# Performance work log

Measured on AMD Instinct MI355X. Metric: run time of the kernel, lower is better.

The kernel has to match this reference:

```python
import jax, jax.numpy as jnp
import numpy as np
from jax import lax

# --- block geometry (matches init_kwargs) ---
B = 8
DIM = 192
HEADS = 6
KEY_DIM = DIM // HEADS  # 32, attn_ratio=1 so d == key_dim and dh == DIM
HX, WX = 32, 32         # search region
HZ, WZ = 16, 16         # template region
T = 1                   # template_number
L = HX * WX + T * HZ * WZ  # 1280 tokens
MLP_HIDDEN = int(DIM * 4.0)
BN_EPS = 1e-5


def _build_bias_idx():
    """Replicates Attention.__init__ global_att=True bias-index construction.
    Unique-offset ids may be permuted vs torch dict-insertion order, which is an
    equivalent reparameterization of the (randomly initialized) bias table."""
    g = np.stack(np.meshgrid(np.arange(HX), np.arange(WX), indexing='ij'), -1).reshape(-1, 2)
    pts = [g]
    for i in range(T):
        r = np.arange(HX + HZ * i, WX + WZ * (i + 1))
        g2 = np.stack(np.meshgrid(r, r, indexing='ij'), -1).reshape(-1, 2)
        pts.append(g2)
    p = np.concatenate(pts, 0)                      # (L, 2)
    off = np.abs(p[:, None, :] - p[None, :, :])     # (L, L, 2)
    key = off[:, :, 0].astype(np.int64) * 4096 + off[:, :, 1]
    uniq, inv = np.unique(key, return_inverse=True)
    return inv.reshape(L, L).astype(np.int32), int(len(uniq))


def setup_inputs() -> dict:
    key = jax.random.key(0)
    ks = jax.random.split(key, 16)
    idx_np, n_off = _build_bias_idx()
    s = 0.02
    return {
        'xz': jax.random.normal(ks[0], (B, L, DIM), jnp.float32),
        'bias_idx': jnp.asarray(idx_np),
        'ln1_g': jnp.ones((DIM,), jnp.float32),
        'ln1_b': jnp.zeros((DIM,), jnp.float32),
        'wqkv': jax.random.normal(ks[1], (DIM, 3 * DIM), jnp.float32) * s,
        'bqkv': jnp.zeros((3 * DIM,), jnp.float32),
        'wproj': jax.random.normal(ks[2], (DIM, DIM), jnp.float32) * s,
        'bproj': jnp.zeros((DIM,), jnp.float32),
        'bias_table': jax.random.normal(ks[3], (HEADS, n_off), jnp.float32) * 0.1,
        'conv_w': jax.random.normal(ks[4], (3, 3, 1, DIM), jnp.float32) * 0.1,  # depthwise HWIO
        'bn_scale': jnp.ones((DIM,), jnp.float32) + jax.random.normal(ks[5], (DIM,), jnp.float32) * 0.01,
        'bn_bias': jax.random.normal(ks[6], (DIM,), jnp.float32) * 0.01,
        'ln2_g': jnp.ones((DIM,), jnp.float32),
        'ln2_b': jnp.zeros((DIM,), jnp.float32),
        'w1': jax.random.normal(ks[7], (DIM, MLP_HIDDEN), jnp.float32) * s,
        'b1': jnp.zeros((MLP_HIDDEN,), jnp.float32),
        'w2': jax.random.normal(ks[8], (MLP_HIDDEN, DIM), jnp.float32) * s,
        'b2': jnp.zeros((DIM,), jnp.float32),
    }


def _layernorm(x, g, b, eps=1e-5):
    mu = jnp.mean(x, -1, keepdims=True)
    var = jnp.mean(jnp.square(x - mu), -1, keepdims=True)
    return (x - mu) * lax.rsqrt(var + eps) * g + b


def reference(xz, bias_idx, ln1_g, ln1_b, wqkv, bqkv, wproj, bproj, bias_table,
              conv_w, bn_scale, bn_bias, ln2_g, ln2_b, w1, b1, w2, b2):
    Bn, N, D = xz.shape
    scale = KEY_DIM ** -0.5
    # --- Attention (LeViT-style with gathered relative-position bias) ---
    h = _layernorm(xz, ln1_g, ln1_b)
    qkv = (h @ wqkv + bqkv).reshape(Bn, N, HEADS, 3 * KEY_DIM)
    q, k, v = jnp.split(qkv, 3, axis=3)            # each (B, N, H, key_dim)
    bias = bias_table[:, bias_idx]                  # (H, N, N) gather
    attn = jnp.einsum('bnhd,bmhd->bhnm', q, k) * scale + bias
    attn = jax.nn.softmax(attn, axis=-1)
    o = jnp.einsum('bhnm,bmhd->bnhd', attn, v).reshape(Bn, N, D)
    xm = xz + o @ wproj + bproj
    # --- depthwise local conv (Conv2d_BN, BN folded to scale/bias) per segment ---
    segs = []
    start = 0
    for (Hh, Ww) in [(HX, WX)] + [(HZ, WZ)] * T:
        xc = xm[:, start:start + Hh * Ww, :].reshape(Bn, Hh, Ww, D)
        xc = lax.conv_general_dilated(
            xc, conv_w, window_strides=(1, 1), padding='SAME',
            dimension_numbers=('NHWC', 'HWIO', 'NHWC'), feature_group_count=D)
        xc = xc * bn_scale + bn_bias
        segs.append(xc.reshape(Bn, Hh * Ww, D))
        start += Hh * Ww
    xm = jnp.concatenate(segs, axis=1)
    # --- MLP with pre-LN (exact GELU, matching nn.GELU default) ---
    m = _layernorm(xm, ln2_g, ln2_b)
    m = jax.nn.gelu(m @ w1 + b1, approximate=False) @ w2 + b2
    return xm + m
```

## Files before the change

kernel.cpp:

```cpp
#include <hip/hip_runtime.h>
#include <hip/hip_bf16.h>

#define BATCH 8
#define LTOK 1280
#define DIMC 192
#define HEADS 6
#define KD 32
#define HID 768
#define NROWS (BATCH*LTOK)

typedef short s16x8 __attribute__((ext_vector_type(8)));
typedef float f32x4 __attribute__((ext_vector_type(4)));
typedef unsigned short u16;

#define QS (0.17677669529663687f * 1.4426950408889634f)
#define L2E 1.4426950408889634f

__device__ __forceinline__ u16 f2bf(float x) {
    unsigned u = __float_as_uint(x);
    u = (u + 0x7FFFu + ((u >> 16) & 1u)) >> 16;
    return (u16)u;
}
__device__ __forceinline__ float bflo(unsigned u) { return __uint_as_float(u << 16); }
__device__ __forceinline__ float bfhi(unsigned u) { return __uint_as_float(u & 0xffff0000u); }
__device__ __forceinline__ float fexp2(float x) { float r; asm("v_exp_f32 %0, %1" : "=v"(r) : "v"(x)); return r; }
__device__ __forceinline__ float frcp(float x)  { float r; asm("v_rcp_f32 %0, %1" : "=v"(r) : "v"(x)); return r; }

__global__ __launch_bounds__(256) void ln_kernel(const float* __restrict__ x,
                                                 const float* __restrict__ g,
                                                 const float* __restrict__ b,
                                                 u16* __restrict__ y) {
    int row = blockIdx.x * 4 + (threadIdx.x >> 6);
    int lane = threadIdx.x & 63;
    const float* xr = x + (size_t)row * DIMC;
    float v0 = xr[lane], v1 = xr[lane + 64], v2 = xr[lane + 128];
    float s = v0 + v1 + v2;
    float ss = v0 * v0 + v1 * v1 + v2 * v2;
    #pragma unroll
    for (int off = 32; off; off >>= 1) {
        s  += __shfl_xor(s, off);
        ss += __shfl_xor(ss, off);
    }
    float mu  = s * (1.0f / DIMC);
    float var = ss * (1.0f / DIMC) - mu * mu;
    float inv = rsqrtf(var + 1e-5f);
    u16* yr = y + (size_t)row * DIMC;
    yr[lane]       = f2bf((v0 - mu) * inv * g[lane]       + b[lane]);
    yr[lane + 64]  = f2bf((v1 - mu) * inv * g[lane + 64]  + b[lane + 64]);
    yr[lane + 128] = f2bf((v2 - mu) * inv * g[lane + 128] + b[lane + 128]);
}

__global__ __launch_bounds__(256) void pre_kernel(const float* w0, const float* w1,
                                                  const float* w2, const float* w3,
                                                  u16* o0, u16* o1, u16* o2, u16* o3,
                                                  const int* __restrict__ bidx,
                                                  const float* __restrict__ btab,
                                                  int n_off, u16* __restrict__ bm) {
    __shared__ float s[16][17];
    int f = blockIdx.x;
    if (f >= 1728) {
        size_t flat = (size_t)(f - 1728) * 1024 + (size_t)threadIdx.x * 4;
        int4 iv = *(const int4*)(bidx + flat);
        #pragma unroll
        for (int h = 0; h < HEADS; ++h) {
            const float* tab = btab + (size_t)h * n_off;
            ushort4 o;
            o.x = f2bf(tab[iv.x] * L2E);
            o.y = f2bf(tab[iv.y] * L2E);
            o.z = f2bf(tab[iv.z] * L2E);
            o.w = f2bf(tab[iv.w] * L2E);
            *(ushort4*)(bm + (size_t)h * (LTOK * LTOK) + flat) = o;
        }
        return;
    }
    const float* in; u16* out; int K, N, tn, tk;
    if (f < 432)       { in = w0; out = o0; K = 192; N = 576; int r = f;        tn = r % 36; tk = r / 36; }
    else if (f < 576)  { in = w1; out = o1; K = 192; N = 192; int r = f - 432;  tn = r % 12; tk = r / 12; }
    else if (f < 1152) { in = w2; out = o2; K = 192; N = 768; int r = f - 576;  tn = r % 48; tk = r / 48; }
    else               { in = w3; out = o3; K = 768; N = 192; int r = f - 1152; tn = r % 12; tk = r / 12; }
    int tx = threadIdx.x & 15, ty = threadIdx.x >> 4;
    s[ty][tx] = in[(size_t)(tk * 16 + ty) * N + tn * 16 + tx];
    __syncthreads();
    out[(size_t)(tn * 16 + ty) * K + tk * 16 + tx] = f2bf(s[tx][ty]);
}

template<int ACT, int RES, int OBF, int QKV, int K, int MTILE>
__global__ __launch_bounds__(256) void gemm_mfma(const u16* __restrict__ A,
                                                 const u16* __restrict__ Wt,
                                                 const float* __restrict__ bias,
                                                 const float* __restrict__ R,
                                                 void* __restrict__ Cp,
                                                 u16* __restrict__ qb,
                                                 u16* __restrict__ kp,
                                                 u16* __restrict__ vp,
                                                 int N) {
    constexpr int SUB = MTILE / 64;
    int tid = threadIdx.x;
    int L = tid & 63, w = tid >> 6;
    int r = L & 15, g = L >> 4;
    int m0 = blockIdx.y * MTILE + w * (16 * SUB);
    int n0 = blockIdx.x * 64;

    f32x4 acc[SUB][4] = {};
    const u16* Ab = A + (size_t)(m0 + r) * K + g * 8;
    const u16* Wb = Wt + (size_t)(n0 + r) * K + g * 8;
    #pragma unroll 6
    for (int k0 = 0; k0 < K; k0 += 32) {
        s16x8 af[SUB];
        #pragma unroll
        for (int mi = 0; mi < SUB; ++mi)
            af[mi] = *(const s16x8*)(Ab + (size_t)mi * 16 * K + k0);
        #pragma unroll
        for (int nn = 0; nn < 4; ++nn) {
            s16x8 bf = *(const s16x8*)(Wb + (size_t)nn * 16 * K + k0);
            #pragma unroll
            for (int mi = 0; mi < SUB; ++mi)
                acc[mi][nn] = __builtin_amdgcn_mfma_f32_16x16x32_bf16(af[mi], bf, acc[mi][nn], 0, 0, 0);
        }
    }

    #pragma unroll
    for (int mi = 0; mi < SUB; ++mi)
    #pragma unroll
    for (int nn = 0; nn < 4; ++nn) {
        int cb = n0 + nn * 16;
        #pragma unroll
        for (int i = 0; i < 4; ++i) {
            int row = m0 + mi * 16 + g * 4 + i;
            float v = acc[mi][nn][i] + bias[cb + r];
            if (QKV) {
                int h  = cb / 96, c0 = cb % 96;
                int reg = c0 >> 5;
                if (reg == 0) {
                    v *= QS;
                    qb[(size_t)row * DIMC + h * 32 + (c0 & 31) + r] = f2bf(v);
                } else {
                    int b_ = row / LTOK, t = row - b_ * LTOK;
                    int T = t >> 5, it = t & 31;
                    int d = (c0 & 31) + r;
                    if (reg == 1) {
                        int which = (it >> 2) & 1;
                        int ik = ((it >> 3) << 2) | (it & 3);
                        int Lk = ((d >> 3) << 4) + ik;
                        kp[((size_t)(b_ * HEADS + h) * 40 + T) * 1024 + which * 512 + Lk * 8 + (d & 7)] = f2bf(v);
                    } else {
                        int Lv = ((it >> 3) << 4) + (d & 15);
                        vp[((size_t)(b_ * HEADS + h) * 40 + T) * 1024 + (d >> 4) * 512 + Lv * 8 + (it & 7)] = f2bf(v);
                    }
                }
            } else {
                if (ACT == 1) {
                    float u = v;
                    float y = 0.7978845608028654f * (u + 0.044715f * u * u * u);
                    float e2 = fexp2(y * 2.885390081777927f);
                    v = u - u * frcp(e2 + 1.0f);
                }
                if (RES) v += R[(size_t)row * N + cb + r];
                if (OBF) ((u16*)Cp)[(size_t)row * N + cb + r] = f2bf(v);
                else     ((float*)Cp)[(size_t)row * N + cb + r] = v;
            }
        }
    }
}

__global__ __launch_bounds__(256) void attn_mfma(const u16* __restrict__ qb,
                                                 const u16* __restrict__ kp,
                                                 const u16* __restrict__ vp,
                                                 const u16* __restrict__ bm,
                                                 u16* __restrict__ ob) {
    __shared__ __align__(16) u16 kvs[3][2][1024];
    int tid = threadIdx.x;
    int L = tid & 63, w = tid >> 6;
    int r = L & 15, g = L >> 4;
    int L8 = L * 8;

    int bid = blockIdx.x;
    int work = (bid & 7) * 120 + (bid >> 3);
    int b  = work & 7;
    int hq = work >> 3;
    int qt = (hq % 20) * 4 + w;
    int h  = hq / 20;

    s16x8 qf = *(const s16x8*)(qb + (size_t)(b * LTOK + qt * 16 + r) * DIMC + h * 32 + g * 8);

    int skv = w >> 1, half = w & 1;
    const u16* gsrc = (skv ? vp : kp) + (size_t)(b * HEADS + h) * 40 * 1024 + half * 512 + L8;
    u16* kvsb = &kvs[0][0][0];
    int dofs = skv * 1024 + half * 512 + L8;

    const u16* bmr = bm + ((size_t)h * LTOK + qt * 16 + r) * LTOK + g * 8;

    f32x4 acc0 = {0.f, 0.f, 0.f, 0.f}, acc1 = {0.f, 0.f, 0.f, 0.f};
    float lsum = 0.f;

    int4 st0 = *(const int4*)(gsrc);
    *(int4*)(kvsb + dofs) = st0;
    int4 sCur = *(const int4*)(gsrc + 1024);
    int4 bv  = *(const int4*)(bmr);
    int4 bvn = *(const int4*)(bmr + 32);
    __syncthreads();

    int rd = 0, wr = 1;
    #pragma unroll 1
    for (int T = 0; T < 40; ++T) {
        int4 sNext, bb;
        if (T < 38) {
            sNext = *(const int4*)(gsrc + (size_t)(T + 2) * 1024);
            bb    = *(const int4*)(bmr + (size_t)(T + 2) * 32);
        }
        u16* bufr = kvsb + rd * 2048;
        f32x4 z0, z1;
        z0[0] = bflo(bv.x); z0[1] = bfhi(bv.x); z0[2] = bflo(bv.y); z0[3] = bfhi(bv.y);
        z1[0] = bflo(bv.z); z1[1] = bfhi(bv.z); z1[2] = bflo(bv.w); z1[3] = bfhi(bv.w);

        s16x8 kf0 = *(const s16x8*)(bufr + L8);
        s16x8 kf1 = *(const s16x8*)(bufr + 512 + L8);
        __builtin_amdgcn_s_setprio(1);
        f32x4 s0 = __builtin_amdgcn_mfma_f32_16x16x32_bf16(kf0, qf, z0, 0, 0, 0);
        f32x4 s1 = __builtin_amdgcn_mfma_f32_16x16x32_bf16(kf1, qf, z1, 0, 0, 0);
        float p[8];
        #pragma unroll
        for (int j = 0; j < 4; ++j) p[j] = fexp2(s0[j]);
        #pragma unroll
        for (int j = 0; j < 4; ++j) p[4 + j] = fexp2(s1[j]);
        lsum += ((p[0] + p[1]) + (p[2] + p[3])) + ((p[4] + p[5]) + (p[6] + p[7]));
        union { unsigned u[4]; s16x8 v; } pbu;
        #pragma unroll
        for (int j = 0; j < 4; ++j)
            asm("v_cvt_pk_bf16_f32 %0, %1, %2" : "=v"(pbu.u[j]) : "v"(p[2 * j]), "v"(p[2 * j + 1]));
        s16x8 v0 = *(const s16x8*)(bufr + 1024 + L8);
        s16x8 v1 = *(const s16x8*)(bufr + 1536 + L8);
        acc0 = __builtin_amdgcn_mfma_f32_16x16x32_bf16(pbu.v, v0, acc0, 0, 0, 0);
        acc1 = __builtin_amdgcn_mfma_f32_16x16x32_bf16(pbu.v, v1, acc1, 0, 0, 0);
        __builtin_amdgcn_s_setprio(0);

        if (T < 39) *(int4*)(kvsb + wr * 2048 + dofs) = sCur;
        __syncthreads();
        sCur = sNext; bv = bvn; bvn = bb;
        rd = wr; wr = (wr == 2) ? 0 : wr + 1;
    }

    float lr = lsum;
    lr += __shfl_xor(lr, 16);
    lr += __shfl_xor(lr, 32);
    #pragma unroll
    for (int i = 0; i < 4; ++i) {
        float linv = frcp(__shfl(lr, 4 * g + i));
        size_t orow = (size_t)(b * LTOK + qt * 16 + 4 * g + i) * DIMC + h * 32 + r;
        ob[orow]      = f2bf(acc0[i] * linv);
        ob[orow + 16] = f2bf(acc1[i] * linv);
    }
}

__global__ __launch_bounds__(256) void conv_ln_kernel(const float* __restrict__ xm,
                                                      const float* __restrict__ w,
                                                      const float* __restrict__ scale,
                                                      const float* __restrict__ bias,
                                                      const float* __restrict__ g2,
                                                      const float* __restrict__ b2,
                                                      float* __restrict__ xm2,
                                                      u16* __restrict__ y) {
    int row = blockIdx.x * 4 + (threadIdx.x >> 6);
    int lane = threadIdx.x & 63;
    int b = row / LTOK, t = row - b * LTOK;
    int H, W, base, y0, x0;
    if (t < 1024) { H = 32; W = 32; base = 0;    y0 = t >> 5;            x0 = t & 31; }
    else          { H = 16; W = 16; base = 1024; int tt = t - 1024; y0 = tt >> 4; x0 = tt & 15; }
    float a0 = 0.f, a1 = 0.f, a2 = 0.f;
    #pragma unroll
    for (int ky = 0; ky < 3; ++ky) {
        int yy = y0 + ky - 1;
        if (yy < 0 || yy >= H) continue;
        #pragma unroll
        for (int kx = 0; kx < 3; ++kx) {
            int xx = x0 + kx - 1;
            if (xx < 0 || xx >= W) continue;
            const float* xr = xm + (size_t)(b * LTOK + base + yy * W + xx) * DIMC;
            const float* wr = w + (ky * 3 + kx) * DIMC;
            a0 += wr[lane]       * xr[lane];
            a1 += wr[lane + 64]  * xr[lane + 64];
            a2 += wr[lane + 128] * xr[lane + 128];
        }
    }
    float v0 = a0 * scale[lane]       + bias[lane];
    float v1 = a1 * scale[lane + 64]  + bias[lane + 64];
    float v2 = a2 * scale[lane + 128] + bias[lane + 128];
    float* xr2 = xm2 + (size_t)row * DIMC;
    xr2[lane] = v0; xr2[lane + 64] = v1; xr2[lane + 128] = v2;
    float s = v0 + v1 + v2;
    float ss = v0 * v0 + v1 * v1 + v2 * v2;
    #pragma unroll
    for (int off = 32; off; off >>= 1) {
        s  += __shfl_xor(s, off);
        ss += __shfl_xor(ss, off);
    }
    float mu  = s * (1.0f / DIMC);
    float var = ss * (1.0f / DIMC) - mu * mu;
    float inv = rsqrtf(var + 1e-5f);
    u16* yr = y + (size_t)row * DIMC;
    yr[lane]       = f2bf((v0 - mu) * inv * g2[lane]       + b2[lane]);
    yr[lane + 64]  = f2bf((v1 - mu) * inv * g2[lane + 64]  + b2[lane + 64]);
    yr[lane + 128] = f2bf((v2 - mu) * inv * g2[lane + 128] + b2[lane + 128]);
}

extern "C" void kernel_launch(void* const* d_in, const int* in_sizes, int n_in,
                              void* d_out, int out_size, void* d_ws, size_t ws_size,
                              hipStream_t stream) {
    const float* xz       = (const float*)d_in[0];
    const int*   bidx     = (const int*)  d_in[1];
    const float* ln1_g    = (const float*)d_in[2];
    const float* ln1_b    = (const float*)d_in[3];
    const float* wqkv     = (const float*)d_in[4];
    const float* bqkv     = (const float*)d_in[5];
    const float* wproj    = (const float*)d_in[6];
    const float* bproj    = (const float*)d_in[7];
    const float* btab     = (const float*)d_in[8];
    const float* conv_w   = (const float*)d_in[9];
    const float* bn_scale = (const float*)d_in[10];
    const float* bn_bias  = (const float*)d_in[11];
    const float* ln2_g    = (const float*)d_in[12];
    const float* ln2_b    = (const float*)d_in[13];
    const float* w1       = (const float*)d_in[14];
    const float* b1       = (const float*)d_in[15];
    const float* w2       = (const float*)d_in[16];
    const float* b2       = (const float*)d_in[17];
    int n_off = in_sizes[8] / HEADS;
    float* out = (float*)d_out;

    char* wsb = (char*)d_ws;
    u16*  hbuf   = (u16*)(wsb + 0);
    u16*  ob     = (u16*)(wsb + 0);
    u16*  wqkvT  = (u16*)(wsb + 3932160);
    u16*  wprojT = (u16*)(wsb + 4153344);
    u16*  w1T    = (u16*)(wsb + 4227072);
    u16*  w2T    = (u16*)(wsb + 4521984);
    u16*  bm     = (u16*)(wsb + 4816896);
    u16*  hid    = (u16*)(wsb + 4816896);
    u16*  kp     = (u16*)(wsb + 24477696);
    u16*  vp     = (u16*)(wsb + 28409856);
    float* xm2   = (float*)(wsb + 24477696);
    u16*  qb     = (u16*)(wsb + 32342016);
    float* xm    = (float*)(wsb + 32342016);

    pre_kernel<<<1728 + LTOK * LTOK / 1024, 256, 0, stream>>>(
        wqkv, wproj, w1, w2, wqkvT, wprojT, w1T, w2T, bidx, btab, n_off, bm);
    ln_kernel<<<NROWS / 4, 256, 0, stream>>>(xz, ln1_g, ln1_b, hbuf);
    gemm_mfma<0,0,0,1,DIMC,128><<<dim3(576 / 64, NROWS / 128), 256, 0, stream>>>(
        hbuf, wqkvT, bqkv, nullptr, nullptr, qb, kp, vp, 3 * DIMC);
    attn_mfma<<<960, 256, 0, stream>>>(qb, kp, vp, bm, ob);
    gemm_mfma<0,1,0,0,DIMC,64><<<dim3(DIMC / 64, NROWS / 64), 256, 0, stream>>>(
        ob, wprojT, bproj, xz, xm, nullptr, nullptr, nullptr, DIMC);
    conv_ln_kernel<<<NROWS / 4, 256, 0, stream>>>(
        xm, conv_w, bn_scale, bn_bias, ln2_g, ln2_b, xm2, hbuf);
    gemm_mfma<1,0,1,0,DIMC,128><<<dim3(HID / 64, NROWS / 128), 256, 0, stream>>>(
        hbuf, w1T, b1, nullptr, hid, nullptr, nullptr, nullptr, HID);
    gemm_mfma<0,1,0,0,HID,128><<<dim3(DIMC / 64, NROWS / 128), 256, 0, stream>>>(
        hid, w2T, b2, xm2, out, nullptr, nullptr, nullptr, DIMC);
}
```

Measured before the change: 136.0 us.

## Fuse LN1 into pre kernel, double KV tile per attention step, retune GEMM tiles

```diff
diff --git a/kernel.cpp b/kernel.cpp
--- a/kernel.cpp
+++ b/kernel.cpp
@@ -26,38 +26,39 @@
 __device__ __forceinline__ float fexp2(float x) { float r; asm("v_exp_f32 %0, %1" : "=v"(r) : "v"(x)); return r; }
 __device__ __forceinline__ float frcp(float x)  { float r; asm("v_rcp_f32 %0, %1" : "=v"(r) : "v"(x)); return r; }
 
-__global__ __launch_bounds__(256) void ln_kernel(const float* __restrict__ x,
-                                                 const float* __restrict__ g,
-                                                 const float* __restrict__ b,
-                                                 u16* __restrict__ y) {
-    int row = blockIdx.x * 4 + (threadIdx.x >> 6);
-    int lane = threadIdx.x & 63;
-    const float* xr = x + (size_t)row * DIMC;
-    float v0 = xr[lane], v1 = xr[lane + 64], v2 = xr[lane + 128];
-    float s = v0 + v1 + v2;
-    float ss = v0 * v0 + v1 * v1 + v2 * v2;
-    #pragma unroll
-    for (int off = 32; off; off >>= 1) {
-        s  += __shfl_xor(s, off);
-        ss += __shfl_xor(ss, off);
-    }
-    float mu  = s * (1.0f / DIMC);
-    float var = ss * (1.0f / DIMC) - mu * mu;
-    float inv = rsqrtf(var + 1e-5f);
-    u16* yr = y + (size_t)row * DIMC;
-    yr[lane]       = f2bf((v0 - mu) * inv * g[lane]       + b[lane]);
-    yr[lane + 64]  = f2bf((v1 - mu) * inv * g[lane + 64]  + b[lane + 64]);
-    yr[lane + 128] = f2bf((v2 - mu) * inv * g[lane + 128] + b[lane + 128]);
-}
-
 __global__ __launch_bounds__(256) void pre_kernel(const float* w0, const float* w1,
                                                   const float* w2, const float* w3,
                                                   u16* o0, u16* o1, u16* o2, u16* o3,
                                                   const int* __restrict__ bidx,
                                                   const float* __restrict__ btab,
-                                                  int n_off, u16* __restrict__ bm) {
+                                                  int n_off, u16* __restrict__ bm,
+                                                  const float* __restrict__ xz,
+                                                  const float* __restrict__ ln1g,
+                                                  const float* __restrict__ ln1b,
+                                                  u16* __restrict__ hbuf) {
     __shared__ float s[16][17];
     int f = blockIdx.x;
+    if (f >= 3328) {
+        int row = (f - 3328) * 4 + (threadIdx.x >> 6);
+        int lane = threadIdx.x & 63;
+        const float* xr = xz + (size_t)row * DIMC;
+        float v0 = xr[lane], v1 = xr[lane + 64], v2 = xr[lane + 128];
+        float sm = v0 + v1 + v2;
+        float ss = v0 * v0 + v1 * v1 + v2 * v2;
+        #pragma unroll
+        for (int off = 32; off; off >>= 1) {
+            sm += __shfl_xor(sm, off);
+            ss += __shfl_xor(ss, off);
+        }
+        float mu  = sm * (1.0f / DIMC);
+        float var = ss * (1.0f / DIMC) - mu * mu;
+        float inv = rsqrtf(var + 1e-5f);
+        u16* yr = hbuf + (size_t)row * DIMC;
+        yr[lane]       = f2bf((v0 - mu) * inv * ln1g[lane]       + ln1b[lane]);
+        yr[lane + 64]  = f2bf((v1 - mu) * inv * ln1g[lane + 64]  + ln1b[lane + 64]);
+        yr[lane + 128] = f2bf((v2 - mu) * inv * ln1g[lane + 128] + ln1b[lane + 128]);
+        return;
+    }
     if (f >= 1728) {
         size_t flat = (size_t)(f - 1728) * 1024 + (size_t)threadIdx.x * 4;
         int4 iv = *(const int4*)(bidx + flat);
@@ -168,7 +169,7 @@
                                                  const u16* __restrict__ vp,
                                                  const u16* __restrict__ bm,
                                                  u16* __restrict__ ob) {
-    __shared__ __align__(16) u16 kvs[3][2][1024];
+    __shared__ __align__(16) u16 kvs[2][2][2048];
     int tid = threadIdx.x;
     int L = tid & 63, w = tid >> 6;
     int r = L & 15, g = L >> 4;
@@ -184,60 +185,85 @@
     s16x8 qf = *(const s16x8*)(qb + (size_t)(b * LTOK + qt * 16 + r) * DIMC + h * 32 + g * 8);
 
     int skv = w >> 1, half = w & 1;
-    const u16* gsrc = (skv ? vp : kp) + (size_t)(b * HEADS + h) * 40 * 1024 + half * 512 + L8;
-    u16* kvsb = &kvs[0][0][0];
-    int dofs = skv * 1024 + half * 512 + L8;
+    const u16* gs = (skv ? vp : kp) + (size_t)(b * HEADS + h) * 40 * 1024 + L8;
+    u16* dst0 = &kvs[0][skv][half * 1024 + L8];
+    u16* dst1 = &kvs[1][skv][half * 1024 + L8];
 
     const u16* bmr = bm + ((size_t)h * LTOK + qt * 16 + r) * LTOK + g * 8;
 
     f32x4 acc0 = {0.f, 0.f, 0.f, 0.f}, acc1 = {0.f, 0.f, 0.f, 0.f};
     float lsum = 0.f;
 
-    int4 st0 = *(const int4*)(gsrc);
-    *(int4*)(kvsb + dofs) = st0;
-    int4 sCur = *(const int4*)(gsrc + 1024);
-    int4 bv  = *(const int4*)(bmr);
-    int4 bvn = *(const int4*)(bmr + 32);
+    {
+        int4 pA = *(const int4*)(gs + half * 1024);
+        int4 pB = *(const int4*)(gs + half * 1024 + 512);
+        *(int4*)dst0 = pA;
+        *(int4*)(dst0 + 512) = pB;
+    }
+    int4 bv0 = *(const int4*)(bmr);
+    int4 bv1 = *(const int4*)(bmr + 32);
     __syncthreads();
 
-    int rd = 0, wr = 1;
     #pragma unroll 1
-    for (int T = 0; T < 40; ++T) {
-        int4 sNext, bb;
-        if (T < 38) {
-            sNext = *(const int4*)(gsrc + (size_t)(T + 2) * 1024);
-            bb    = *(const int4*)(bmr + (size_t)(T + 2) * 32);
-        }
-        u16* bufr = kvsb + rd * 2048;
-        f32x4 z0, z1;
-        z0[0] = bflo(bv.x); z0[1] = bfhi(bv.x); z0[2] = bflo(bv.y); z0[3] = bfhi(bv.y);
-        z1[0] = bflo(bv.z); z1[1] = bfhi(bv.z); z1[2] = bflo(bv.w); z1[3] = bfhi(bv.w);
-
-        s16x8 kf0 = *(const s16x8*)(bufr + L8);
-        s16x8 kf1 = *(const s16x8*)(bufr + 512 + L8);
+    for (int T = 0; T < 20; ++T) {
+        int4 nA, nB, nb0, nb1;
+        if (T < 19) {
+            nA  = *(const int4*)(gs + (size_t)(2 * T + 2 + half) * 1024);
+            nB  = *(const int4*)(gs + (size_t)(2 * T + 2 + half) * 1024 + 512);
+            nb0 = *(const int4*)(bmr + (size_t)(T + 1) * 64);
+            nb1 = *(const int4*)(bmr + (size_t)(T + 1) * 64 + 32);
+        }
+        const u16* kb = &kvs[T & 1][0][0];
+        const u16* vb = &kvs[T & 1][1][0];
+        f32x4 z0, z1, z2, z3;
+        z0[0] = bflo(bv0.x); z0[1] = bfhi(bv0.x); z0[2] = bflo(bv0.y); z0[3] = bfhi(bv0.y);
+        z1[0] = bflo(bv0.z); z1[1] = bfhi(bv0.z); z1[2] = bflo(bv0.w); z1[3] = bfhi(bv0.w);
+        z2[0] = bflo(bv1.x); z2[1] = bfhi(bv1.x); z2[2] = bflo(bv1.y); z2[3] = bfhi(bv1.y);
+        z3[0] = bflo(bv1.z); z3[1] = bfhi(bv1.z); z3[2] = bflo(bv1.w); z3[3] = bfhi(bv1.w);
+
+        s16x8 kf0 = *(const s16x8*)(kb + L8);
+        s16x8 kf1 = *(const s16x8*)(kb + 512 + L8);
+        s16x8 kf2 = *(const s16x8*)(kb + 1024 + L8);
+        s16x8 kf3 = *(const s16x8*)(kb + 1536 + L8);
         __builtin_amdgcn_s_setprio(1);
         f32x4 s0 = __builtin_amdgcn_mfma_f32_16x16x32_bf16(kf0, qf, z0, 0, 0, 0);
         f32x4 s1 = __builtin_amdgcn_mfma_f32_16x16x32_bf16(kf1, qf, z1, 0, 0, 0);
-        float p[8];
-        #pragma unroll
-        for (int j = 0; j < 4; ++j) p[j] = fexp2(s0[j]);
-        #pragma unroll
-        for (int j = 0; j < 4; ++j) p[4 + j] = fexp2(s1[j]);
-        lsum += ((p[0] + p[1]) + (p[2] + p[3])) + ((p[4] + p[5]) + (p[6] + p[7]));
-        union { unsigned u[4]; s16x8 v; } pbu;
-        #pragma unroll
-        for (int j = 0; j < 4; ++j)
-            asm("v_cvt_pk_bf16_f32 %0, %1, %2" : "=v"(pbu.u[j]) : "v"(p[2 * j]), "v"(p[2 * j + 1]));
-        s16x8 v0 = *(const s16x8*)(bufr + 1024 + L8);
-        s16x8 v1 = *(const s16x8*)(bufr + 1536 + L8);
-        acc0 = __builtin_amdgcn_mfma_f32_16x16x32_bf16(pbu.v, v0, acc0, 0, 0, 0);
-        acc1 = __builtin_amdgcn_mfma_f32_16x16x32_bf16(pbu.v, v1, acc1, 0, 0, 0);
+        f32x4 s2 = __builtin_amdgcn_mfma_f32_16x16x32_bf16(kf2, qf, z2, 0, 0, 0);
+        f32x4 s3 = __builtin_amdgcn_mfma_f32_16x16x32_bf16(kf3, qf, z3, 0, 0, 0);
+        float p[16];
+        #pragma unroll
+        for (int j = 0; j < 4; ++j) {
+            p[j]      = fexp2(s0[j]);
+            p[4 + j]  = fexp2(s1[j]);
+            p[8 + j]  = fexp2(s2[j]);
+            p[12 + j] = fexp2(s3[j]);
+        }
+        float t0 = ((p[0] + p[1]) + (p[2] + p[3])) + ((p[4] + p[5]) + (p[6] + p[7]));
+        float t1 = ((p[8] + p[9]) + (p[10] + p[11])) + ((p[12] + p[13]) + (p[14] + p[15]));
+        lsum += t0 + t1;
+        union { unsigned u[4]; s16x8 v; } pa, pb;
+        #pragma unroll
+        for (int j = 0; j < 4; ++j) {
+            asm("v_cvt_pk_bf16_f32 %0, %1, %2" : "=v"(pa.u[j]) : "v"(p[2 * j]), "v"(p[2 * j + 1]));
+            asm("v_cvt_pk_bf16_f32 %0, %1, %2" : "=v"(pb.u[j]) : "v"(p[8 + 2 * j]), "v"(p[9 + 2 * j]));
+        }
+        s16x8 v0 = *(const s16x8*)(vb + L8);
+        s16x8 v1 = *(const s16x8*)(vb + 512 + L8);
+        s16x8 v2 = *(const s16x8*)(vb + 1024 + L8);
+        s16x8 v3 = *(const s16x8*)(vb + 1536 + L8);
+        acc0 = __builtin_amdgcn_mfma_f32_16x16x32_bf16(pa.v, v0, acc0, 0, 0, 0);
+        acc1 = __builtin_amdgcn_mfma_f32_16x16x32_bf16(pa.v, v1, acc1, 0, 0, 0);
+        acc0 = __builtin_amdgcn_mfma_f32_16x16x32_bf16(pb.v, v2, acc0, 0, 0, 0);
+        acc1 = __builtin_amdgcn_mfma_f32_16x16x32_bf16(pb.v, v3, acc1, 0, 0, 0);
         __builtin_amdgcn_s_setprio(0);
 
-        if (T < 39) *(int4*)(kvsb + wr * 2048 + dofs) = sCur;
+        if (T < 19) {
+            u16* d = (T & 1) ? dst0 : dst1;
+            *(int4*)d = nA;
+            *(int4*)(d + 512) = nB;
+            bv0 = nb0; bv1 = nb1;
+        }
         __syncthreads();
-        sCur = sNext; bv = bvn; bvn = bb;
-        rd = wr; wr = (wr == 2) ? 0 : wr + 1;
     }
 
     float lr = lsum;
@@ -342,17 +368,17 @@
     u16*  qb     = (u16*)(wsb + 32342016);
     float* xm    = (float*)(wsb + 32342016);
 
-    pre_kernel<<<1728 + LTOK * LTOK / 1024, 256, 0, stream>>>(
-        wqkv, wproj, w1, w2, wqkvT, wprojT, w1T, w2T, bidx, btab, n_off, bm);
-    ln_kernel<<<NROWS / 4, 256, 0, stream>>>(xz, ln1_g, ln1_b, hbuf);
-    gemm_mfma<0,0,0,1,DIMC,128><<<dim3(576 / 64, NROWS / 128), 256, 0, stream>>>(
+    pre_kernel<<<1728 + LTOK * LTOK / 1024 + NROWS / 4, 256, 0, stream>>>(
+        wqkv, wproj, w1, w2, wqkvT, wprojT, w1T, w2T, bidx, btab, n_off, bm,
+        xz, ln1_g, ln1_b, hbuf);
+    gemm_mfma<0,0,0,1,DIMC,256><<<dim3(576 / 64, NROWS / 256), 256, 0, stream>>>(
         hbuf, wqkvT, bqkv, nullptr, nullptr, qb, kp, vp, 3 * DIMC);
     attn_mfma<<<960, 256, 0, stream>>>(qb, kp, vp, bm, ob);
-    gemm_mfma<0,1,0,0,DIMC,64><<<dim3(DIMC / 64, NROWS / 64), 256, 0, stream>>>(
+    gemm_mfma<0,1,0,0,DIMC,128><<<dim3(DIMC / 64, NROWS / 128), 256, 0, stream>>>(
         ob, wprojT, bproj, xz, xm, nullptr, nullptr, nullptr, DIMC);
     conv_ln_kernel<<<NROWS / 4, 256, 0, stream>>>(
         xm, conv_w, bn_scale, bn_bias, ln2_g, ln2_b, xm2, hbuf);
-    gemm_mfma<1,0,1,0,DIMC,128><<<dim3(HID / 64, NROWS / 128), 256, 0, stream>>>(
+    gemm_mfma<1,0,1,0,DIMC,256><<<dim3(HID / 64, NROWS / 256), 256, 0, stream>>>(
         hbuf, w1T, b1, nullptr, hid, nullptr, nullptr, nullptr, HID);
     gemm_mfma<0,1,0,0,HID,128><<<dim3(DIMC / 64, NROWS / 128), 256, 0, stream>>>(
         hid, w2T, b2, xm2, out, nullptr, nullptr, nullptr, DIMC);
```

Measured after the change: 128.9 us. 5.3% less time.
